# Performance work log

Hardware: AMD Instinct MI355X
Metric: run time of the kernel (lower is better)

## Reference

```python
import jax, jax.numpy as jnp
import numpy as np

N = 20000      # nodes
E = 320000     # edges (avg degree 16)
IN, HID, OUT, H = 128, 32, 32, 8
NEG_SLOPE = 0.2


def _gat_conv(x, src, dst, W, al, ar, b):
    """One DGL-style GATConv. x: [N, F_in], W: [F_in, H*D], al/ar: [H, D], b: [H*D].
    Returns [N, H, D]."""
    n = x.shape[0]
    Hh, D = al.shape
    feat = (x @ W).reshape(n, Hh, D)                      # [N,H,D]
    el = jnp.sum(feat * al[None], axis=-1)                # [N,H]
    er = jnp.sum(feat * ar[None], axis=-1)                # [N,H]
    e = jax.nn.leaky_relu(el[src] + er[dst], NEG_SLOPE)   # [E,H]
    # edge softmax over incoming edges of each dst node (stable)
    emax = jax.ops.segment_max(e, dst, num_segments=n)    # [N,H]
    ee = jnp.exp(e - emax[dst])                           # [E,H]
    denom = jax.ops.segment_sum(ee, dst, num_segments=n)  # [N,H]
    alpha = ee / denom[dst]                               # [E,H]
    msg = feat[src] * alpha[:, :, None]                   # [E,H,D] gather+weight
    out = jax.ops.segment_sum(msg, dst, num_segments=n)   # [N,H,D] scatter-add
    return out + b.reshape(1, Hh, D)


def setup_inputs() -> dict:
    key = jax.random.key(0)
    ks = jax.random.split(key, 11)
    return {
        "x":   jax.random.normal(ks[0], (N, IN), dtype=jnp.float32),
        "src": jax.random.randint(ks[1], (E,), 0, N, dtype=jnp.int32),
        "dst": jax.random.randint(ks[2], (E,), 0, N, dtype=jnp.int32),
        "W1":  jax.random.normal(ks[3], (IN, H * HID), dtype=jnp.float32) * 0.1,
        "al1": jax.random.normal(ks[4], (H, HID), dtype=jnp.float32) * 0.1,
        "ar1": jax.random.normal(ks[5], (H, HID), dtype=jnp.float32) * 0.1,
        "b1":  jnp.zeros((H * HID,), dtype=jnp.float32),
        "W2":  jax.random.normal(ks[6], (HID, H * OUT), dtype=jnp.float32) * 0.1,
        "al2": jax.random.normal(ks[7], (H, OUT), dtype=jnp.float32) * 0.1,
        "ar2": jax.random.normal(ks[8], (H, OUT), dtype=jnp.float32) * 0.1,
        "b2":  jnp.zeros((H * OUT,), dtype=jnp.float32),
    }


def reference(x, src, dst, W1, al1, ar1, b1, W2, al2, ar2, b2):
    h = _gat_conv(x, src, dst, W1, al1, ar1, b1)          # [N,H,HID]
    h = jnp.mean(jax.nn.relu(h), axis=1)                  # [N,HID]
    h = _gat_conv(h, src, dst, W2, al2, ar2, b2)          # [N,H,OUT]
    return jnp.mean(h, axis=1)                            # [N,OUT]
```

## Files before the change

kernel.cpp:

```cpp
#include <hip/hip_runtime.h>
#include <hip/hip_bf16.h>

#define N_NODES 20000
#define N_EDGES 320000
#define F_IN    128
#define F_HID   32
#define NHEAD   8
#define FDIM    256
#define CAP     96

#define GROUPS  313
#define GPAD    16
#define GCAP    2048
#define EPB     2048
#define P1B     ((N_EDGES + EPB - 1) / EPB)

#define TW2     12

typedef __hip_bfloat16 bf16;
typedef __attribute__((ext_vector_type(8))) short short8;
typedef __attribute__((ext_vector_type(4))) float f32x4;

__device__ __forceinline__ unsigned short f2bf_rne(float f){
  unsigned u = __float_as_uint(f);
  unsigned r = u + 0x7FFFu + ((u >> 16) & 1u);
  return (unsigned short)(r >> 16);
}
__device__ __forceinline__ float bf2f(unsigned short s){
  return __uint_as_float((unsigned)s << 16);
}

__global__ void init_kernel(const float* __restrict__ W1, const float* __restrict__ W2,
                            const float* __restrict__ al2, const float* __restrict__ ar2,
                            int* __restrict__ gcnt,
                            unsigned short* __restrict__ h1, unsigned short* __restrict__ l1,
                            float* __restrict__ q_lt, float* __restrict__ q_rt){
  const int b = blockIdx.x;
  if (b == 0){
    for (int i = threadIdx.x; i < GROUPS*GPAD; i += 256) gcnt[i] = 0;
  } else if (b < 129){
    int i = (b - 1)*256 + threadIdx.x;
    int n = i >> 7, k = i & 127;
    float v = W1[(size_t)k*FDIM + n];
    unsigned short hs = f2bf_rne(v);
    h1[i] = hs;
    l1[i] = f2bf_rne(v - bf2f(hs));
  } else {
    int t = threadIdx.x;
    int k = t >> 3, hh = t & 7;
    float sl = 0.f, sr = 0.f;
    #pragma unroll
    for (int d = 0; d < 32; d++){
      float w = W2[(size_t)k*FDIM + hh*32 + d];
      sl = fmaf(w, al2[hh*32 + d], sl);
      sr = fmaf(w, ar2[hh*32 + d], sr);
    }
    q_lt[t] = sl;
    q_rt[t] = sr;
  }
}

#define GEMMB  (N_NODES / 16)
__global__ __launch_bounds__(256) void gemm_p1_kernel(
    const int* __restrict__ src, const int* __restrict__ dst,
    int* __restrict__ gcnt, unsigned* __restrict__ recs,
    const float* __restrict__ X,
    const unsigned short* __restrict__ Wthi, const unsigned short* __restrict__ Wtlo,
    const float* __restrict__ al, const float* __restrict__ ar,
    unsigned short* __restrict__ feat, float* __restrict__ el, float* __restrict__ er)
{
  const int b = blockIdx.x;
  const int tid = threadIdx.x;

  if (b < P1B){
    __shared__ int hist[GROUPS];
    for (int t = tid; t < GROUPS; t += 256) hist[t] = 0;
    __syncthreads();

    unsigned rec[8]; int bin[8]; bool val[8];
    const int e0 = b * EPB;
    #pragma unroll
    for (int k = 0; k < 8; k++){
      int i = e0 + k*256 + tid;
      val[k] = (i < N_EDGES);
      if (val[k]){
        int s = src[i];
        int d = dst[i];
        bin[k] = d >> 6;
        rec[k] = (unsigned)(((d & 63) << 16) | s);
        atomicAdd(&hist[bin[k]], 1);
      }
    }
    __syncthreads();
    {
      const int rot = (b * 97) % GROUPS;
      for (int tt = tid; tt < GROUPS; tt += 256){
        int t = tt + rot; if (t >= GROUPS) t -= GROUPS;
        int h = hist[t];
        hist[t] = (h > 0) ? atomicAdd(&gcnt[t*GPAD], h) : 0;
      }
    }
    __syncthreads();
    #pragma unroll
    for (int k = 0; k < 8; k++){
      if (val[k]){
        int pos = atomicAdd(&hist[bin[k]], 1);
        if (pos < GCAP) recs[(size_t)bin[k]*GCAP + pos] = rec[k];
      }
    }
    return;
  }

  constexpr int K = F_IN;
  const int wv   = tid >> 6;
  const int lane = tid & 63;
  const int quad = lane >> 4;
  const int l16  = lane & 15;
  const int m0   = (b - P1B) * 16;
  constexpr int NC = K / 32;

  short8 Ah[NC], Al_[NC];
  {
    const float* xrow = X + (size_t)(m0 + l16)*K;
    #pragma unroll
    for (int c = 0; c < NC; c++){
      float4 a0 = *(const float4*)(xrow + c*32 + quad*8);
      float4 a1 = *(const float4*)(xrow + c*32 + quad*8 + 4);
      const float vs[8] = {a0.x,a0.y,a0.z,a0.w,a1.x,a1.y,a1.z,a1.w};
      #pragma unroll
      for (int j = 0; j < 8; j++){
        unsigned short hs = f2bf_rne(vs[j]);
        Ah[c][j]  = (short)hs;
        Al_[c][j] = (short)f2bf_rne(vs[j] - bf2f(hs));
      }
    }
  }

  float elp[8], erp[8];
  #pragma unroll
  for (int j = 0; j < 8; j++){ elp[j] = 0.f; erp[j] = 0.f; }

  #pragma unroll
  for (int t = 0; t < 4; t++){
    const int nc = wv*64 + t*16;
    const size_t brow = (size_t)(nc + l16) * K;
    f32x4 acc = {0.f, 0.f, 0.f, 0.f};
    #pragma unroll
    for (int c = 0; c < NC; c++){
      short8 Bh = *(const short8*)(Wthi + brow + c*32 + quad*8);
      short8 Bl = *(const short8*)(Wtlo + brow + c*32 + quad*8);
      acc = __builtin_amdgcn_mfma_f32_16x16x32_bf16(Ah[c],  Bh, acc, 0, 0, 0);
      acc = __builtin_amdgcn_mfma_f32_16x16x32_bf16(Ah[c],  Bl, acc, 0, 0, 0);
      acc = __builtin_amdgcn_mfma_f32_16x16x32_bf16(Al_[c], Bh, acc, 0, 0, 0);
    }
    const float alv = al[nc + l16];
    const float arv = ar[nc + l16];
    const int hl = t >> 1;
    #pragma unroll
    for (int r = 0; r < 4; r++){
      float v = acc[r];
      feat[(size_t)(m0 + quad*4 + r)*FDIM + nc + l16] = f2bf_rne(v);
      elp[r*2 + hl] = fmaf(v, alv, elp[r*2 + hl]);
      erp[r*2 + hl] = fmaf(v, arv, erp[r*2 + hl]);
    }
  }

  #pragma unroll
  for (int off = 1; off <= 8; off <<= 1){
    #pragma unroll
    for (int j = 0; j < 8; j++){
      elp[j] += __shfl_xor(elp[j], off);
      erp[j] += __shfl_xor(erp[j], off);
    }
  }
  __shared__ float el_lds[16][8], er_lds[16][8];
  if (l16 == 0){
    #pragma unroll
    for (int r = 0; r < 4; r++){
      #pragma unroll
      for (int hl = 0; hl < 2; hl++){
        el_lds[quad*4 + r][wv*2 + hl] = elp[r*2 + hl];
        er_lds[quad*4 + r][wv*2 + hl] = erp[r*2 + hl];
      }
    }
  }
  __syncthreads();
  if (tid < 128){
    int row = tid >> 3, h = tid & 7;
    el[(size_t)(m0 + row)*NHEAD + h] = el_lds[row][h];
    er[(size_t)(m0 + row)*NHEAD + h] = er_lds[row][h];
  }
}

__global__ __launch_bounds__(256) void bucket_build_kernel(
    const unsigned* __restrict__ recs, const int* __restrict__ gcnt,
    int* __restrict__ cnt, int* __restrict__ bucket)
{
  const int g  = blockIdx.x;
  const int n0 = g << 6;
  __shared__ int lcnt[64];
  __shared__ int lbuck[64*CAP];
  if (threadIdx.x < 64) lcnt[threadIdx.x] = 0;
  __syncthreads();

  int m = gcnt[g*GPAD]; if (m > GCAP) m = GCAP;
  for (int r = threadIdx.x; r < m; r += 256){
    unsigned w = recs[(size_t)g*GCAP + r];
    int d = (int)(w >> 16);
    int p = atomicAdd(&lcnt[d], 1);
    if (p < CAP) lbuck[d*CAP + p] = (int)(w & 0xFFFFu);
  }
  __syncthreads();

  int nn = N_NODES - n0; if (nn > 64) nn = 64;
  if (threadIdx.x < nn) cnt[n0 + threadIdx.x] = lcnt[threadIdx.x];
  const int tot4 = (nn * CAP) >> 2;
  int4* gb = (int4*)(bucket + (size_t)n0 * CAP);
  const int4* lb = (const int4*)lbuck;
  for (int i = threadIdx.x; i < tot4; i += 256) gb[i] = lb[i];
}

__global__ __launch_bounds__(256) void edge_agg_l1(
    const bf16* __restrict__ feat, const float* __restrict__ el,
    const float* __restrict__ er, const int* __restrict__ cnt,
    const int* __restrict__ bucket, const float* __restrict__ bias,
    const float* __restrict__ q_lt, const float* __restrict__ q_rt,
    unsigned short* __restrict__ h_out, float* __restrict__ el2,
    float* __restrict__ er2)
{
  const int tid  = threadIdx.x;
  const int wv   = tid >> 6;
  const int lane = tid & 63;
  const int n    = blockIdx.x*4 + wv;

  __shared__ float t_all[4][CAP*9];
  __shared__ int   s_all[4][CAP];
  __shared__ float sum_all[4][NHEAD];
  __shared__ float v_all[4][256];
  float* t_w = t_all[wv];
  int*   s_w = s_all[wv];

  int C = cnt[n];
  if (C > CAP) C = CAP;

  const float4* er4 = (const float4*)(er + (size_t)n*NHEAD);
  float4 era = er4[0], erb = er4[1];
  const float erv[8] = {era.x, era.y, era.z, era.w, erb.x, erb.y, erb.z, erb.w};

  for (int idx = lane; idx < C*2; idx += 64){
    const int e = idx >> 1, j = idx & 1;
    const int sidx = bucket[(size_t)n*CAP + e];
    if (j == 0) s_w[e] = sidx;
    float4 a = ((const float4*)(el + (size_t)sidx*NHEAD))[j];
    const float ev[4] = {a.x, a.y, a.z, a.w};
    #pragma unroll
    for (int hh = 0; hh < 4; hh++){
      float v = ev[hh] + erv[j*4 + hh];
      t_w[e*9 + j*4 + hh] = (v > 0.f) ? v : 0.2f*v;
    }
  }
  {
    const int h = lane >> 3, d = lane & 7;
    float lm = -INFINITY;
    for (int e = d; e < C; e += 8) lm = fmaxf(lm, t_w[e*9 + h]);
    #pragma unroll
    for (int off = 4; off >= 1; off >>= 1) lm = fmaxf(lm, __shfl_xor(lm, off));
    float ls = 0.f;
    for (int e = d; e < C; e += 8){
      float ex = __expf(t_w[e*9 + h] - lm);
      t_w[e*9 + h] = ex;
      ls += ex;
    }
    #pragma unroll
    for (int off = 4; off >= 1; off >>= 1) ls += __shfl_xor(ls, off);
    if (d == 0) sum_all[wv][h] = ls;
  }

  const int sub = lane >> 5;
  const int l   = lane & 31;
  const int hB  = l >> 2;
  const int coff = l << 3;
  float acc[8] = {0,0,0,0,0,0,0,0};
  int e = sub;
  float4 fv0, fv1;
  if (e < C)     fv0 = *(const float4*)(feat + (size_t)s_w[e]*FDIM + coff);
  if (e + 2 < C) fv1 = *(const float4*)(feat + (size_t)s_w[e+2]*FDIM + coff);
  while (e < C){
    float4 fnext;
    if (e + 4 < C) fnext = *(const float4*)(feat + (size_t)s_w[e+4]*FDIM + coff);
    const float w = t_w[e*9 + hB];
    const unsigned* u = (const unsigned*)&fv0;
    #pragma unroll
    for (int j = 0; j < 4; j++){
      float flo = __uint_as_float(u[j] << 16);
      float fhi = __uint_as_float(u[j] & 0xFFFF0000u);
      acc[2*j]   = fmaf(w, flo, acc[2*j]);
      acc[2*j+1] = fmaf(w, fhi, acc[2*j+1]);
    }
    fv0 = fv1; fv1 = fnext;
    e += 2;
  }
  #pragma unroll
  for (int j = 0; j < 8; j++) acc[j] += __shfl_xor(acc[j], 32);

  if (lane < 32){
    const float s = sum_all[wv][l >> 2];
    const float4* b4 = (const float4*)(bias + coff);
    float4 ba = b4[0], bb = b4[1];
    float bv[8] = {ba.x, ba.y, ba.z, ba.w, bb.x, bb.y, bb.z, bb.w};
    float v[8];
    #pragma unroll
    for (int j = 0; j < 8; j++){
      float val = (C > 0) ? (acc[j] / s) : 0.f;
      val += bv[j];
      val = fmaxf(val, 0.f);
      v[j] = val;
    }
    float4* v4 = (float4*)&v_all[wv][coff];
    v4[0] = make_float4(v[0], v[1], v[2], v[3]);
    v4[1] = make_float4(v[4], v[5], v[6], v[7]);
  }
  if (lane < 32){
    float hsum = 0.f;
    #pragma unroll
    for (int hh = 0; hh < 8; hh++) hsum += v_all[wv][hh*32 + lane];
    hsum *= 0.125f;
    h_out[(size_t)n*32 + lane] = f2bf_rne(hsum);

    float4 qa0 = ((const float4*)(q_lt + lane*8))[0];
    float4 qa1 = ((const float4*)(q_lt + lane*8))[1];
    float4 qb0 = ((const float4*)(q_rt + lane*8))[0];
    float4 qb1 = ((const float4*)(q_rt + lane*8))[1];
    float pl[8] = {hsum*qa0.x, hsum*qa0.y, hsum*qa0.z, hsum*qa0.w,
                   hsum*qa1.x, hsum*qa1.y, hsum*qa1.z, hsum*qa1.w};
    float pr[8] = {hsum*qb0.x, hsum*qb0.y, hsum*qb0.z, hsum*qb0.w,
                   hsum*qb1.x, hsum*qb1.y, hsum*qb1.z, hsum*qb1.w};
    #pragma unroll
    for (int off = 1; off <= 16; off <<= 1){
      #pragma unroll
      for (int j = 0; j < 8; j++){
        pl[j] += __shfl_xor(pl[j], off);
        pr[j] += __shfl_xor(pr[j], off);
      }
    }
    if (l == 0){
      #pragma unroll
      for (int j = 0; j < 8; j++){
        el2[(size_t)n*NHEAD + j] = pl[j];
        er2[(size_t)n*NHEAD + j] = pr[j];
      }
    }
  }
}

__global__ __launch_bounds__(256) void edge_agg_l2(
    const unsigned short* __restrict__ h_bf, const float* __restrict__ el2,
    const float* __restrict__ er2, const int* __restrict__ cnt,
    const int* __restrict__ bucket, const float* __restrict__ W2,
    const float* __restrict__ b2, float* __restrict__ outp)
{
  const int tid  = threadIdx.x;
  const int wv   = tid >> 6;
  const int lane = tid & 63;
  const int n    = blockIdx.x*4 + wv;

  __shared__ __align__(16) float t_all[4][CAP*TW2];
  __shared__ int   s_all[4][CAP];
  __shared__ float sum_all[4][NHEAD];
  __shared__ float A_lds[4][NHEAD][33];
  __shared__ float red[4][256];
  float* t_w = t_all[wv];
  int*   s_w = s_all[wv];

  int C = cnt[n];
  if (C > CAP) C = CAP;

  const float4* er4 = (const float4*)(er2 + (size_t)n*NHEAD);
  float4 era = er4[0], erb = er4[1];
  const float erv[8] = {era.x, era.y, era.z, era.w, erb.x, erb.y, erb.z, erb.w};

  for (int idx = lane; idx < C*2; idx += 64){
    const int e = idx >> 1, j = idx & 1;
    const int sidx = bucket[(size_t)n*CAP + e];
    if (j == 0) s_w[e] = sidx;
    float4 a = ((const float4*)(el2 + (size_t)sidx*NHEAD))[j];
    const float ev[4] = {a.x, a.y, a.z, a.w};
    #pragma unroll
    for (int hh = 0; hh < 4; hh++){
      float v = ev[hh] + erv[j*4 + hh];
      t_w[e*TW2 + j*4 + hh] = (v > 0.f) ? v : 0.2f*v;
    }
  }
  {
    const int h = lane >> 3, d = lane & 7;
    float lm = -INFINITY;
    for (int e = d; e < C; e += 8) lm = fmaxf(lm, t_w[e*TW2 + h]);
    #pragma unroll
    for (int off = 4; off >= 1; off >>= 1) lm = fmaxf(lm, __shfl_xor(lm, off));
    float ls = 0.f;
    for (int e = d; e < C; e += 8){
      float ex = __expf(t_w[e*TW2 + h] - lm);
      t_w[e*TW2 + h] = ex;
      ls += ex;
    }
    #pragma unroll
    for (int off = 4; off >= 1; off >>= 1) ls += __shfl_xor(ls, off);
    if (d == 0) sum_all[wv][h] = ls;
  }

  const int sub = lane >> 4;
  const int q   = lane & 15;
  float acc[16];
  #pragma unroll
  for (int i = 0; i < 16; i++) acc[i] = 0.f;
  int e = sub;
  unsigned hv;
  if (e < C) hv = *(const unsigned*)(h_bf + (size_t)s_w[e]*32 + q*2);
  while (e < C){
    const int en = e + 4;
    unsigned hnext;
    if (en < C) hnext = *(const unsigned*)(h_bf + (size_t)s_w[en]*32 + q*2);
    f32x4 w0 = *(const f32x4*)&t_w[e*TW2];
    f32x4 w1 = *(const f32x4*)&t_w[e*TW2 + 4];
    const float x0 = __uint_as_float(hv << 16);
    const float x1 = __uint_as_float(hv & 0xFFFF0000u);
    #pragma unroll
    for (int h = 0; h < 4; h++){
      acc[2*h]   = fmaf(w0[h], x0, acc[2*h]);
      acc[2*h+1] = fmaf(w0[h], x1, acc[2*h+1]);
      acc[8+2*h]   = fmaf(w1[h], x0, acc[8+2*h]);
      acc[8+2*h+1] = fmaf(w1[h], x1, acc[8+2*h+1]);
    }
    hv = hnext;
    e = en;
  }
  #pragma unroll
  for (int i = 0; i < 16; i++){
    acc[i] += __shfl_xor(acc[i], 16);
    acc[i] += __shfl_xor(acc[i], 32);
  }
  if (lane < 16){
    #pragma unroll
    for (int h = 0; h < 8; h++){
      const float s = sum_all[wv][h];
      const float inv = (C > 0) ? (1.f / s) : 0.f;
      A_lds[wv][h][2*lane]     = acc[2*h]   * inv;
      A_lds[wv][h][2*lane + 1] = acc[2*h+1] * inv;
    }
  }
  __syncthreads();

  {
    const int c  = tid;
    const int hc = c >> 5;
    float p0=0.f, p1=0.f, p2=0.f, p3=0.f;
    for (int k = 0; k < F_HID; k++){
      float w = W2[(size_t)k*FDIM + c];
      p0 = fmaf(A_lds[0][hc][k], w, p0);
      p1 = fmaf(A_lds[1][hc][k], w, p1);
      p2 = fmaf(A_lds[2][hc][k], w, p2);
      p3 = fmaf(A_lds[3][hc][k], w, p3);
    }
    red[0][c] = p0; red[1][c] = p1; red[2][c] = p2; red[3][c] = p3;
  }
  __syncthreads();
  if (tid < 128){
    const int nn = tid >> 5, d = tid & 31;
    float s = 0.f, bm = 0.f;
    #pragma unroll
    for (int hh = 0; hh < 8; hh++){
      s  += red[nn][hh*32 + d];
      bm += b2[hh*32 + d];
    }
    outp[(size_t)(blockIdx.x*4 + nn)*32 + d] = (s + bm) * 0.125f;
  }
}

extern "C" void kernel_launch(void* const* d_in, const int* in_sizes, int n_in,
                              void* d_out, int out_size, void* d_ws, size_t ws_size,
                              hipStream_t stream)
{
  const float* x   = (const float*)d_in[0];
  const int*   src = (const int*)  d_in[1];
  const int*   dst = (const int*)  d_in[2];
  const float* W1  = (const float*)d_in[3];
  const float* al1 = (const float*)d_in[4];
  const float* ar1 = (const float*)d_in[5];
  const float* b1  = (const float*)d_in[6];
  const float* W2  = (const float*)d_in[7];
  const float* al2 = (const float*)d_in[8];
  const float* ar2 = (const float*)d_in[9];
  const float* b2  = (const float*)d_in[10];
  (void)in_sizes; (void)n_in; (void)out_size; (void)ws_size;

  size_t o = 0;
  char* base = (char*)d_ws;
  auto take = [&](size_t bytes) -> char* {
    char* p = base + o;
    o += (bytes + 255) & ~(size_t)255;
    return p;
  };
  unsigned short* feat  = (unsigned short*)take((size_t)N_NODES*FDIM*2);
  float* el1    = (float*)take((size_t)N_NODES*NHEAD*4);
  float* er1    = (float*)take((size_t)N_NODES*NHEAD*4);
  float* el2    = (float*)take((size_t)N_NODES*NHEAD*4);
  float* er2    = (float*)take((size_t)N_NODES*NHEAD*4);
  int*   cnt    = (int*)  take((size_t)N_NODES*4);
  int*   bucket = (int*)  take((size_t)N_NODES*CAP*4);
  unsigned short* hbf  = (unsigned short*)take((size_t)N_NODES*F_HID*2);
  unsigned short* W1th = (unsigned short*)take((size_t)FDIM*F_IN*2);
  unsigned short* W1tl = (unsigned short*)take((size_t)FDIM*F_IN*2);
  float* q_lt   = (float*)take((size_t)F_HID*NHEAD*4);
  float* q_rt   = (float*)take((size_t)F_HID*NHEAD*4);
  int*   gcnt   = (int*)  take((size_t)GROUPS*GPAD*4);
  unsigned* recs = (unsigned*)take((size_t)GROUPS*GCAP*4);

  init_kernel<<<130, 256, 0, stream>>>(
      W1, W2, al2, ar2, gcnt, W1th, W1tl, q_lt, q_rt);

  gemm_p1_kernel<<<P1B + GEMMB, 256, 0, stream>>>(
      src, dst, gcnt, recs, x, W1th, W1tl, al1, ar1, feat, el1, er1);

  bucket_build_kernel<<<GROUPS, 256, 0, stream>>>(recs, gcnt, cnt, bucket);

  edge_agg_l1<<<N_NODES/4, 256, 0, stream>>>(
      (const bf16*)feat, el1, er1, cnt, bucket, b1, q_lt, q_rt, hbf, el2, er2);

  edge_agg_l2<<<N_NODES/4, 256, 0, stream>>>(
      hbf, el2, er2, cnt, bucket, W2, b2, (float*)d_out);
}
```

Before: 182.9 us.

## Shrink edge aggregation LDS footprint and use single-wave blocks for layer 1

```diff
diff --git a/kernel.cpp b/kernel.cpp
--- a/kernel.cpp
+++ b/kernel.cpp
@@ -220,7 +220,7 @@
   for (int i = threadIdx.x; i < tot4; i += 256) gb[i] = lb[i];
 }
 
-__global__ __launch_bounds__(256) void edge_agg_l1(
+__global__ __launch_bounds__(64, 6) void edge_agg_l1(
     const bf16* __restrict__ feat, const float* __restrict__ el,
     const float* __restrict__ er, const int* __restrict__ cnt,
     const int* __restrict__ bucket, const float* __restrict__ bias,
@@ -228,17 +228,14 @@
     unsigned short* __restrict__ h_out, float* __restrict__ el2,
     float* __restrict__ er2)
 {
-  const int tid  = threadIdx.x;
-  const int wv   = tid >> 6;
-  const int lane = tid & 63;
-  const int n    = blockIdx.x*4 + wv;
-
-  __shared__ float t_all[4][CAP*9];
-  __shared__ int   s_all[4][CAP];
-  __shared__ float sum_all[4][NHEAD];
-  __shared__ float v_all[4][256];
-  float* t_w = t_all[wv];
-  int*   s_w = s_all[wv];
+  const int lane = threadIdx.x;
+  const int n    = blockIdx.x;
+
+  __shared__ float t_w[CAP*9];
+  __shared__ int   s_w[CAP];
+  __shared__ float sum_h[NHEAD];
+  __shared__ float v_sh[256];
+  __shared__ float h_sh[32];
 
   int C = cnt[n];
   if (C > CAP) C = CAP;
@@ -273,7 +270,7 @@
     }
     #pragma unroll
     for (int off = 4; off >= 1; off >>= 1) ls += __shfl_xor(ls, off);
-    if (d == 0) sum_all[wv][h] = ls;
+    if (d == 0) sum_h[h] = ls;
   }
 
   const int sub = lane >> 5;
@@ -304,7 +301,7 @@
   for (int j = 0; j < 8; j++) acc[j] += __shfl_xor(acc[j], 32);
 
   if (lane < 32){
-    const float s = sum_all[wv][l >> 2];
+    const float s = sum_h[lane >> 2];
     const float4* b4 = (const float4*)(bias + coff);
     float4 ba = b4[0], bb = b4[1];
     float bv[8] = {ba.x, ba.y, ba.z, ba.w, bb.x, bb.y, bb.z, bb.w};
@@ -316,44 +313,36 @@
       val = fmaxf(val, 0.f);
       v[j] = val;
     }
-    float4* v4 = (float4*)&v_all[wv][coff];
+    float4* v4 = (float4*)&v_sh[coff];
     v4[0] = make_float4(v[0], v[1], v[2], v[3]);
     v4[1] = make_float4(v[4], v[5], v[6], v[7]);
   }
   if (lane < 32){
     float hsum = 0.f;
     #pragma unroll
-    for (int hh = 0; hh < 8; hh++) hsum += v_all[wv][hh*32 + lane];
+    for (int hh = 0; hh < 8; hh++) hsum += v_sh[hh*32 + lane];
     hsum *= 0.125f;
     h_out[(size_t)n*32 + lane] = f2bf_rne(hsum);
-
-    float4 qa0 = ((const float4*)(q_lt + lane*8))[0];
-    float4 qa1 = ((const float4*)(q_lt + lane*8))[1];
-    float4 qb0 = ((const float4*)(q_rt + lane*8))[0];
-    float4 qb1 = ((const float4*)(q_rt + lane*8))[1];
-    float pl[8] = {hsum*qa0.x, hsum*qa0.y, hsum*qa0.z, hsum*qa0.w,
-                   hsum*qa1.x, hsum*qa1.y, hsum*qa1.z, hsum*qa1.w};
-    float pr[8] = {hsum*qb0.x, hsum*qb0.y, hsum*qb0.z, hsum*qb0.w,
-                   hsum*qb1.x, hsum*qb1.y, hsum*qb1.z, hsum*qb1.w};
-    #pragma unroll
-    for (int off = 1; off <= 16; off <<= 1){
-      #pragma unroll
-      for (int j = 0; j < 8; j++){
-        pl[j] += __shfl_xor(pl[j], off);
-        pr[j] += __shfl_xor(pr[j], off);
-      }
-    }
-    if (l == 0){
-      #pragma unroll
-      for (int j = 0; j < 8; j++){
-        el2[(size_t)n*NHEAD + j] = pl[j];
-        er2[(size_t)n*NHEAD + j] = pr[j];
-      }
-    }
-  }
-}
-
-__global__ __launch_bounds__(256) void edge_agg_l2(
+    h_sh[lane] = hsum;
+  }
+  if (lane < 32){
+    const int j    = lane & 7;
+    const int sel  = (lane >> 3) & 1;
+    const int half = lane >> 4;
+    const float* qt = sel ? q_rt : q_lt;
+    float p = 0.f;
+    #pragma unroll
+    for (int k = 0; k < 16; k++){
+      const int kk = half*16 + k;
+      p = fmaf(h_sh[kk], qt[kk*8 + j], p);
+    }
+    p += __shfl_xor(p, 16);
+    if (lane < 8)       el2[(size_t)n*NHEAD + j] = p;
+    else if (lane < 16) er2[(size_t)n*NHEAD + j] = p;
+  }
+}
+
+__global__ __launch_bounds__(256, 6) void edge_agg_l2(
     const unsigned short* __restrict__ h_bf, const float* __restrict__ el2,
     const float* __restrict__ er2, const int* __restrict__ cnt,
     const int* __restrict__ bucket, const float* __restrict__ W2,
@@ -367,8 +356,6 @@
   __shared__ __align__(16) float t_all[4][CAP*TW2];
   __shared__ int   s_all[4][CAP];
   __shared__ float sum_all[4][NHEAD];
-  __shared__ float A_lds[4][NHEAD][33];
-  __shared__ float red[4][256];
   float* t_w = t_all[wv];
   int*   s_w = s_all[wv];
 
@@ -444,8 +431,8 @@
     for (int h = 0; h < 8; h++){
       const float s = sum_all[wv][h];
       const float inv = (C > 0) ? (1.f / s) : 0.f;
-      A_lds[wv][h][2*lane]     = acc[2*h]   * inv;
-      A_lds[wv][h][2*lane + 1] = acc[2*h+1] * inv;
+      t_w[h*33 + 2*lane]     = acc[2*h]   * inv;
+      t_w[h*33 + 2*lane + 1] = acc[2*h+1] * inv;
     }
   }
   __syncthreads();
@@ -456,12 +443,15 @@
     float p0=0.f, p1=0.f, p2=0.f, p3=0.f;
     for (int k = 0; k < F_HID; k++){
       float w = W2[(size_t)k*FDIM + c];
-      p0 = fmaf(A_lds[0][hc][k], w, p0);
-      p1 = fmaf(A_lds[1][hc][k], w, p1);
-      p2 = fmaf(A_lds[2][hc][k], w, p2);
-      p3 = fmaf(A_lds[3][hc][k], w, p3);
-    }
-    red[0][c] = p0; red[1][c] = p1; red[2][c] = p2; red[3][c] = p3;
+      p0 = fmaf(t_all[0][hc*33 + k], w, p0);
+      p1 = fmaf(t_all[1][hc*33 + k], w, p1);
+      p2 = fmaf(t_all[2][hc*33 + k], w, p2);
+      p3 = fmaf(t_all[3][hc*33 + k], w, p3);
+    }
+    t_all[0][512 + c] = p0;
+    t_all[1][512 + c] = p1;
+    t_all[2][512 + c] = p2;
+    t_all[3][512 + c] = p3;
   }
   __syncthreads();
   if (tid < 128){
@@ -469,7 +459,7 @@
     float s = 0.f, bm = 0.f;
     #pragma unroll
     for (int hh = 0; hh < 8; hh++){
-      s  += red[nn][hh*32 + d];
+      s  += t_all[nn][512 + hh*32 + d];
       bm += b2[hh*32 + d];
     }
     outp[(size_t)(blockIdx.x*4 + nn)*32 + d] = (s + bm) * 0.125f;
@@ -523,7 +513,7 @@
 
   bucket_build_kernel<<<GROUPS, 256, 0, stream>>>(recs, gcnt, cnt, bucket);
 
-  edge_agg_l1<<<N_NODES/4, 256, 0, stream>>>(
+  edge_agg_l1<<<N_NODES, 64, 0, stream>>>(
       (const bf16*)feat, el1, er1, cnt, bucket, b1, q_lt, q_rt, hbf, el2, er2);
 
   edge_agg_l2<<<N_NODES/4, 256, 0, stream>>>(
```

Result: faster. 170.3 us (-6.9%).
